# Kernel optimization log

Measured on AMD Instinct MI355X. Metric: run time of the kernel, lower is better.

Reference implementation:

```python
import jax, jax.numpy as jnp
import numpy as np
import math

ROPE_BASE = 10000.0
ALIBI_SLOPE = 2.0 ** (-8.0)  # _get_alibi_slopes(1) == [2**(-8*1/1)]


def _rope_cos_sin(T, d):
    inv_freq = 1.0 / (ROPE_BASE ** (jnp.arange(0, d, 2, dtype=jnp.float32) / d))
    t = jnp.arange(T, dtype=jnp.float32)
    freqs = jnp.einsum('i,j->ij', t, inv_freq)          # [T, d/2]
    emb = jnp.concatenate([freqs, freqs], axis=-1)      # [T, d]
    return jnp.cos(emb), jnp.sin(emb)


def _rotate_half(x):
    x1, x2 = jnp.split(x, 2, axis=-1)
    return jnp.concatenate([-x2, x1], axis=-1)


def setup_inputs() -> dict:
    key = jax.random.key(0)
    kq, kk, kv = jax.random.split(key, 3)
    B, T, H = 8, 2048, 256
    return {
        'q': jax.random.normal(kq, (B, T, H), dtype=jnp.float32),
        'k': jax.random.normal(kk, (B, T, H), dtype=jnp.float32),
        'v': jax.random.normal(kv, (B, T, H), dtype=jnp.float32),
    }


def reference(q, k, v):
    B, T, H = q.shape  # num_heads == 1, so head_dim == H
    cos, sin = _rope_cos_sin(T, H)                      # [T, H]
    qe = q * cos + _rotate_half(q) * sin                # [B, T, H]
    ke = k * cos + _rotate_half(k) * sin                # [B, T, H]

    scale = 1.0 / math.sqrt(H)
    scores = jnp.einsum('btd,bsd->bts', qe, ke) * scale  # [B, T, T]

    pos = jnp.arange(T)
    rel = (pos[None, :] - pos[:, None]).astype(jnp.float32)  # [T, T]
    alibi = (ALIBI_SLOPE * rel)[None, None, :, :]            # [1, 1, T, T]

    # torch broadcast: [B,T,T] + [1,1,T,T] -> [1,B,T,T]
    scores = scores + alibi
    attn = jax.nn.softmax(scores, axis=-1)              # [1, B, T, T]
    out = jnp.matmul(attn, v)                           # [1, B, T, H]
    return out
```

## Files before the change

### kernel.cpp

```cpp
#include <hip/hip_runtime.h>

#define B_ 8
#define T_ 2048
#define H_ 256
#define PSTR 40
#define SCALE2 0.0901684403f
#define SLOPE2 0.00563552752f
#define ELEMS ((size_t)B_ * T_ * H_)

typedef __attribute__((ext_vector_type(8))) short bf16x8;
typedef __attribute__((ext_vector_type(4))) float f32x4;

#define MFMA16(a, b, c) __builtin_amdgcn_mfma_f32_16x16x32_bf16((a), (b), (c), 0, 0, 0)

__device__ __forceinline__ ushort f2bf(float f) {
  unsigned u = __float_as_uint(f);
  u += 0x7FFFu + ((u >> 16) & 1u);
  return (ushort)(u >> 16);
}

__device__ __forceinline__ void gl_lds16(const ushort* g, ushort* l) {
  __builtin_amdgcn_global_load_lds(
      (const __attribute__((address_space(1))) unsigned int*)g,
      (__attribute__((address_space(3))) unsigned int*)l, 16, 0, 0);
}

__global__ void prep_kernel(const float* __restrict__ k, const float* __restrict__ v,
                            ushort* __restrict__ kt, ushort* __restrict__ vt) {
  __shared__ ushort tile[64][72];
  const int bid = blockIdx.x;
  const int tid = threadIdx.x;
  if (bid < 1024) {
    int idx = bid * 256 + tid;
    int d8 = idx & 15;
    int bt = idx >> 4;
    int t = bt & (T_ - 1);
    int b = bt >> 11;
    size_t base = (size_t)bt * H_ + d8 * 8;
    float4 a0 = *(const float4*)(k + base);
    float4 a1 = *(const float4*)(k + base + 4);
    float4 c0 = *(const float4*)(k + base + 128);
    float4 c1 = *(const float4*)(k + base + 132);
    float av[8] = {a0.x, a0.y, a0.z, a0.w, a1.x, a1.y, a1.z, a1.w};
    float cv[8] = {c0.x, c0.y, c0.z, c0.w, c1.x, c1.y, c1.z, c1.w};
    bf16x8 lo, hi;
#pragma unroll
    for (int e = 0; e < 8; ++e) {
      int j = d8 * 8 + e;
      float rv = (float)t * exp2f((float)j * -0.103810252959f) * 0.15915494309f;
      float fr = rv - floorf(rv);
      float sn = __builtin_amdgcn_sinf(fr), cs = __builtin_amdgcn_cosf(fr);
      lo[e] = (short)f2bf(av[e] * cs - cv[e] * sn);
      hi[e] = (short)f2bf(cv[e] * cs + av[e] * sn);
    }
    size_t kdst = (((size_t)(b * 64 + (t >> 5)) * 32 + d8) * 32 + (t & 31)) * 8;
    *(bf16x8*)(kt + kdst) = lo;
    *(bf16x8*)(kt + kdst + 4096) = hi;
  } else {
    int bid2 = bid - 1024;
    int b = bid2 >> 7, rem = bid2 & 127;
    int h0 = (rem >> 5) * 64, t0 = (rem & 31) * 64;
    int c4 = tid & 15, r0 = tid >> 4;
#pragma unroll
    for (int p = 0; p < 4; ++p) {
      int row = r0 + p * 16;
      const float4 f = *(const float4*)(v + ((size_t)(b * T_ + t0 + row)) * H_ + h0 + c4 * 4);
      ushort4 u;
      u.x = f2bf(f.x); u.y = f2bf(f.y); u.z = f2bf(f.z); u.w = f2bf(f.w);
      *(ushort4*)&tile[row][(c4 * 4) ^ (8 * ((row >> 3) & 7))] = u;
    }
    __syncthreads();
#pragma unroll
    for (int p = 0; p < 2; ++p) {
      int c = tid + p * 256;
      int h = c >> 3, tc = (c & 7) * 8;
      int xo = 8 * (c & 7);
      ushort4 u0, u1;
      u0.x = tile[tc + 0][h ^ xo]; u0.y = tile[tc + 1][h ^ xo];
      u0.z = tile[tc + 2][h ^ xo]; u0.w = tile[tc + 3][h ^ xo];
      u1.x = tile[tc + 4][h ^ xo]; u1.y = tile[tc + 5][h ^ xo];
      u1.z = tile[tc + 6][h ^ xo]; u1.w = tile[tc + 7][h ^ xo];
      int tg = t0 + tc;
      size_t dst = (((size_t)(b * 64 + (tg >> 5)) * 4 + ((tg >> 3) & 3)) * 256 + (h0 + h)) * 8;
      *(ushort4*)(vt + dst) = u0;
      *(ushort4*)(vt + dst + 4) = u1;
    }
  }
}

__global__ __launch_bounds__(256, 2)
void attn_kernel(const float* __restrict__ q, const ushort* __restrict__ kt,
                 const ushort* __restrict__ vt, float* __restrict__ out,
                 float* __restrict__ opart, float* __restrict__ lpart) {
  __shared__ ushort Ksh[2][8192];
  __shared__ ushort Vsh[2][8192];
  __shared__ ushort Psh[4][32 * PSTR];

  const int tid = threadIdx.x;
  const int w = tid >> 6, lane = tid & 63, quad = lane >> 4, l16 = lane & 15;
  const int b = blockIdx.x;
  const int q0 = blockIdx.y * 128;
  const int sp = blockIdx.z;
  const int S = gridDim.z;
  const int niter = (T_ / 32) / S;
  const int kvb = sp * (T_ / S);

  bf16x8 aq[2][8];
  {
    const float* qb = q + ((size_t)(b * T_) + q0 + w * 32) * H_;
#pragma unroll
    for (int mt = 0; mt < 2; ++mt) {
      int t = q0 + w * 32 + mt * 16 + l16;
      float qv[8][8];
#pragma unroll
      for (int ks = 0; ks < 8; ++ks) {
        float4 x0 = *(const float4*)(qb + (size_t)(mt * 16 + l16) * H_ + ks * 32 + quad * 8);
        float4 x1 = *(const float4*)(qb + (size_t)(mt * 16 + l16) * H_ + ks * 32 + quad * 8 + 4);
        qv[ks][0] = x0.x; qv[ks][1] = x0.y; qv[ks][2] = x0.z; qv[ks][3] = x0.w;
        qv[ks][4] = x1.x; qv[ks][5] = x1.y; qv[ks][6] = x1.z; qv[ks][7] = x1.w;
      }
#pragma unroll
      for (int ks = 0; ks < 4; ++ks)
#pragma unroll
        for (int e = 0; e < 8; ++e) {
          int d = ks * 32 + quad * 8 + e;
          float rv = (float)t * exp2f((float)d * -0.103810252959f) * 0.15915494309f;
          float fr = rv - floorf(rv);
          float sn = __builtin_amdgcn_sinf(fr), cs = __builtin_amdgcn_cosf(fr);
          aq[mt][ks][e]     = (short)f2bf(qv[ks][e] * cs - qv[ks + 4][e] * sn);
          aq[mt][ks + 4][e] = (short)f2bf(qv[ks + 4][e] * cs + qv[ks][e] * sn);
        }
    }
  }

  const f32x4 fzero = {0.f, 0.f, 0.f, 0.f};
  f32x4 O[2][16], lac[2];
#pragma unroll
  for (int mt = 0; mt < 2; ++mt) {
    lac[mt] = fzero;
#pragma unroll
    for (int ht = 0; ht < 16; ++ht) O[mt][ht] = fzero;
  }
  bf16x8 vones;
#pragma unroll
  for (int i = 0; i < 8; ++i) vones[i] = (short)0x3F80;

  const ushort* ktb = kt + (size_t)(b * 64 + sp * niter) * 8192;
  const ushort* vtb = vt + (size_t)(b * 64 + sp * niter) * 8192;
  const int stoff = tid * 8;

#pragma unroll
  for (int tt = 0; tt < 2; ++tt) {
    const ushort* kg = ktb + (size_t)tt * 8192;
    const ushort* vg = vtb + (size_t)tt * 8192;
#pragma unroll
    for (int i = 0; i < 4; ++i) {
      gl_lds16(kg + stoff + i * 2048, &Ksh[tt][stoff + i * 2048]);
      gl_lds16(vg + stoff + i * 2048, &Vsh[tt][stoff + i * 2048]);
    }
  }

  const float arb = SLOPE2 * (float)(q0 + w * 32 + quad * 4);

  for (int it = 0; it < niter; ++it) {
    const int p = it & 1;
    __builtin_amdgcn_sched_barrier(0);
    if (it == niter - 1) __builtin_amdgcn_s_waitcnt(0x0070);
    else                 __builtin_amdgcn_s_waitcnt(0x0F78);
    __builtin_amdgcn_s_barrier();
    __builtin_amdgcn_sched_barrier(0);

    f32x4 s[2][2] = {{fzero, fzero}, {fzero, fzero}};
    __builtin_amdgcn_s_setprio(1);
#pragma unroll
    for (int ks = 0; ks < 8; ++ks)
#pragma unroll
      for (int nt = 0; nt < 2; ++nt) {
        bf16x8 kf = *(const bf16x8*)&Ksh[p][((ks * 4 + quad) * 32 + nt * 16 + l16) * 8];
        s[0][nt] = MFMA16(aq[0][ks], kf, s[0][nt]);
        s[1][nt] = MFMA16(aq[1][ks], kf, s[1][nt]);
      }
    __builtin_amdgcn_s_setprio(0);

#pragma unroll
    for (int nt = 0; nt < 2; ++nt) {
      float ac = SLOPE2 * (float)(kvb + it * 32 + nt * 16 + l16);
#pragma unroll
      for (int mt = 0; mt < 2; ++mt)
#pragma unroll
        for (int r = 0; r < 4; ++r) {
          float a0 = ac - arb - SLOPE2 * (float)(mt * 16 + r);
          float pv = __builtin_amdgcn_exp2f(fmaf(s[mt][nt][r], SCALE2, a0));
          Psh[w][(mt * 16 + quad * 4 + r) * PSTR + nt * 16 + l16] = f2bf(pv);
        }
    }

    bf16x8 pf0 = *(const bf16x8*)&Psh[w][l16 * PSTR + quad * 8];
    bf16x8 pf1 = *(const bf16x8*)&Psh[w][(16 + l16) * PSTR + quad * 8];
    __builtin_amdgcn_s_setprio(1);
    lac[0] = MFMA16(pf0, vones, lac[0]);
    lac[1] = MFMA16(pf1, vones, lac[1]);
#pragma unroll
    for (int ht = 0; ht < 16; ++ht) {
      bf16x8 vf = *(const bf16x8*)&Vsh[p][(quad * 256 + ht * 16 + l16) * 8];
      O[0][ht] = MFMA16(pf0, vf, O[0][ht]);
      O[1][ht] = MFMA16(pf1, vf, O[1][ht]);
    }
    __builtin_amdgcn_s_setprio(0);

    __builtin_amdgcn_sched_barrier(0);
    __builtin_amdgcn_s_waitcnt(0xC07F);
    __builtin_amdgcn_s_barrier();
    __builtin_amdgcn_sched_barrier(0);

    if (it < niter - 2) {
      const ushort* kg = ktb + (size_t)(it + 2) * 8192;
      const ushort* vg = vtb + (size_t)(it + 2) * 8192;
#pragma unroll
      for (int i = 0; i < 4; ++i) {
        gl_lds16(kg + stoff + i * 2048, &Ksh[p][stoff + i * 2048]);
        gl_lds16(vg + stoff + i * 2048, &Vsh[p][stoff + i * 2048]);
      }
    }
  }

  float* od = (sp == 0) ? out : (opart + (size_t)(sp - 1) * ELEMS);
  float* ob = od + ((size_t)(b * T_) + q0 + w * 32) * H_;
#pragma unroll
  for (int mt = 0; mt < 2; ++mt)
#pragma unroll
    for (int r = 0; r < 4; ++r) {
      int row = mt * 16 + quad * 4 + r;
#pragma unroll
      for (int ht = 0; ht < 16; ++ht)
        ob[(size_t)row * H_ + ht * 16 + l16] = O[mt][ht][r];
    }
  if (l16 == 0) {
#pragma unroll
    for (int mt = 0; mt < 2; ++mt)
#pragma unroll
      for (int r = 0; r < 4; ++r)
        lpart[(size_t)(sp * B_ + b) * T_ + q0 + w * 32 + mt * 16 + quad * 4 + r] =
            lac[mt][r];
  }
}

__global__ void combine_kernel(float* __restrict__ out, const float* __restrict__ opart,
                               const float* __restrict__ lpart, int S) {
  int idx = blockIdx.x * 256 + threadIdx.x;
  int row = idx >> 6;
  float l = lpart[row];
  for (int s = 1; s < S; ++s) l += lpart[(size_t)s * B_ * T_ + row];
  float inv = 1.0f / l;
  float4 a = ((const float4*)out)[idx];
  for (int s = 1; s < S; ++s) {
    float4 c = ((const float4*)opart)[(size_t)(s - 1) * (ELEMS / 4) + idx];
    a.x += c.x; a.y += c.y; a.z += c.z; a.w += c.w;
  }
  a.x *= inv; a.y *= inv; a.z *= inv; a.w *= inv;
  ((float4*)out)[idx] = a;
}

extern "C" void kernel_launch(void* const* d_in, const int* in_sizes, int n_in,
                              void* d_out, int out_size, void* d_ws, size_t ws_size,
                              hipStream_t stream) {
  const float* q = (const float*)d_in[0];
  const float* k = (const float*)d_in[1];
  const float* v = (const float*)d_in[2];
  float* out = (float*)d_out;

  ushort* kt = (ushort*)d_ws;
  ushort* vt = kt + ELEMS;
  float* opart = (float*)(vt + ELEMS);
  const size_t need4 = ELEMS * 4 + 3 * ELEMS * 4 + (size_t)4 * B_ * T_ * 4;
  const int S = (ws_size >= need4) ? 4 : 2;
  float* lpart = opart + (size_t)(S - 1) * ELEMS;

  prep_kernel<<<dim3(2048), 256, 0, stream>>>(k, v, kt, vt);
  attn_kernel<<<dim3(B_, T_ / 128, S), 256, 0, stream>>>(q, kt, vt, out, opart, lpart);
  combine_kernel<<<dim3((B_ * T_ * H_ / 4) / 256), 256, 0, stream>>>(out, opart, lpart, S);
}
```

Before: 152.3 us.

## Software-pipeline QK^T one tile ahead of softmax/PV and fix split to two

Restructures the attention loop so that the QK^T MFMAs for tile it are issued in the same iteration as the exp/PV work for tile it-1, using a triple-buffered V tile in LDS so V stays resident one extra iteration. The KV split is hardcoded to 2 (down from 4 when workspace allowed), which shrinks the combine pass and partial-output traffic but halves grid parallelism. Launch bounds drop to 1 block per CU to give the extra live accumulators registers, and setprio hints are removed. The risk is reduced occupancy and fewer blocks (256 total) hurting latency hiding on a 256-CU part.

```diff
diff --git a/kernel.cpp b/kernel.cpp
--- a/kernel.cpp
+++ b/kernel.cpp
@@ -88,12 +88,12 @@
   }
 }
 
-__global__ __launch_bounds__(256, 2)
+__global__ __launch_bounds__(256, 1)
 void attn_kernel(const float* __restrict__ q, const ushort* __restrict__ kt,
                  const ushort* __restrict__ vt, float* __restrict__ out,
-                 float* __restrict__ opart, float* __restrict__ lpart) {
+                 float* __restrict__ o1, float* __restrict__ lpart) {
   __shared__ ushort Ksh[2][8192];
-  __shared__ ushort Vsh[2][8192];
+  __shared__ ushort Vsh[3][8192];
   __shared__ ushort Psh[4][32 * PSTR];
 
   const int tid = threadIdx.x;
@@ -101,9 +101,7 @@
   const int b = blockIdx.x;
   const int q0 = blockIdx.y * 128;
   const int sp = blockIdx.z;
-  const int S = gridDim.z;
-  const int niter = (T_ / 32) / S;
-  const int kvb = sp * (T_ / S);
+  const int kvb = sp * (T_ / 2);
 
   bf16x8 aq[2][8];
   {
@@ -145,8 +143,8 @@
 #pragma unroll
   for (int i = 0; i < 8; ++i) vones[i] = (short)0x3F80;
 
-  const ushort* ktb = kt + (size_t)(b * 64 + sp * niter) * 8192;
-  const ushort* vtb = vt + (size_t)(b * 64 + sp * niter) * 8192;
+  const ushort* ktb = kt + (size_t)(b * 64 + sp * 32) * 8192;
+  const ushort* vtb = vt + (size_t)(b * 64 + sp * 32) * 8192;
   const int stoff = tid * 8;
 
 #pragma unroll
@@ -161,70 +159,125 @@
   }
 
   const float arb = SLOPE2 * (float)(q0 + w * 32 + quad * 4);
-
-  for (int it = 0; it < niter; ++it) {
+  f32x4 s_prev[2][2] = {{fzero, fzero}, {fzero, fzero}};
+
+  {
+    __builtin_amdgcn_sched_barrier(0);
+    __builtin_amdgcn_s_waitcnt(0x0F78);
+    __builtin_amdgcn_s_barrier();
+    __builtin_amdgcn_sched_barrier(0);
+#pragma unroll
+    for (int ks = 0; ks < 8; ++ks)
+#pragma unroll
+      for (int nt = 0; nt < 2; ++nt) {
+        bf16x8 kf = *(const bf16x8*)&Ksh[0][((ks * 4 + quad) * 32 + nt * 16 + l16) * 8];
+        s_prev[0][nt] = MFMA16(aq[0][ks], kf, s_prev[0][nt]);
+        s_prev[1][nt] = MFMA16(aq[1][ks], kf, s_prev[1][nt]);
+      }
+    __builtin_amdgcn_sched_barrier(0);
+    __builtin_amdgcn_s_waitcnt(0xC07F);
+    __builtin_amdgcn_s_barrier();
+    __builtin_amdgcn_sched_barrier(0);
+    const ushort* kg = ktb + (size_t)2 * 8192;
+    const ushort* vg = vtb + (size_t)2 * 8192;
+#pragma unroll
+    for (int i = 0; i < 4; ++i) {
+      gl_lds16(kg + stoff + i * 2048, &Ksh[0][stoff + i * 2048]);
+      gl_lds16(vg + stoff + i * 2048, &Vsh[2][stoff + i * 2048]);
+    }
+  }
+
+  for (int it = 1; it < 32; ++it) {
     const int p = it & 1;
-    __builtin_amdgcn_sched_barrier(0);
-    if (it == niter - 1) __builtin_amdgcn_s_waitcnt(0x0070);
-    else                 __builtin_amdgcn_s_waitcnt(0x0F78);
+    const int vp = (it - 1) % 3;
+    __builtin_amdgcn_sched_barrier(0);
+    if (it == 31) __builtin_amdgcn_s_waitcnt(0x0070);
+    else          __builtin_amdgcn_s_waitcnt(0x0F78);
     __builtin_amdgcn_s_barrier();
     __builtin_amdgcn_sched_barrier(0);
 
-    f32x4 s[2][2] = {{fzero, fzero}, {fzero, fzero}};
-    __builtin_amdgcn_s_setprio(1);
+    f32x4 s_cur[2][2] = {{fzero, fzero}, {fzero, fzero}};
 #pragma unroll
     for (int ks = 0; ks < 8; ++ks)
 #pragma unroll
       for (int nt = 0; nt < 2; ++nt) {
         bf16x8 kf = *(const bf16x8*)&Ksh[p][((ks * 4 + quad) * 32 + nt * 16 + l16) * 8];
-        s[0][nt] = MFMA16(aq[0][ks], kf, s[0][nt]);
-        s[1][nt] = MFMA16(aq[1][ks], kf, s[1][nt]);
+        s_cur[0][nt] = MFMA16(aq[0][ks], kf, s_cur[0][nt]);
+        s_cur[1][nt] = MFMA16(aq[1][ks], kf, s_cur[1][nt]);
       }
-    __builtin_amdgcn_s_setprio(0);
 
 #pragma unroll
     for (int nt = 0; nt < 2; ++nt) {
-      float ac = SLOPE2 * (float)(kvb + it * 32 + nt * 16 + l16);
+      float ac = SLOPE2 * (float)(kvb + (it - 1) * 32 + nt * 16 + l16);
 #pragma unroll
       for (int mt = 0; mt < 2; ++mt)
 #pragma unroll
         for (int r = 0; r < 4; ++r) {
           float a0 = ac - arb - SLOPE2 * (float)(mt * 16 + r);
-          float pv = __builtin_amdgcn_exp2f(fmaf(s[mt][nt][r], SCALE2, a0));
+          float pv = __builtin_amdgcn_exp2f(fmaf(s_prev[mt][nt][r], SCALE2, a0));
           Psh[w][(mt * 16 + quad * 4 + r) * PSTR + nt * 16 + l16] = f2bf(pv);
         }
     }
 
     bf16x8 pf0 = *(const bf16x8*)&Psh[w][l16 * PSTR + quad * 8];
     bf16x8 pf1 = *(const bf16x8*)&Psh[w][(16 + l16) * PSTR + quad * 8];
-    __builtin_amdgcn_s_setprio(1);
     lac[0] = MFMA16(pf0, vones, lac[0]);
     lac[1] = MFMA16(pf1, vones, lac[1]);
 #pragma unroll
     for (int ht = 0; ht < 16; ++ht) {
-      bf16x8 vf = *(const bf16x8*)&Vsh[p][(quad * 256 + ht * 16 + l16) * 8];
+      bf16x8 vf = *(const bf16x8*)&Vsh[vp][(quad * 256 + ht * 16 + l16) * 8];
       O[0][ht] = MFMA16(pf0, vf, O[0][ht]);
       O[1][ht] = MFMA16(pf1, vf, O[1][ht]);
     }
-    __builtin_amdgcn_s_setprio(0);
+
+#pragma unroll
+    for (int mt = 0; mt < 2; ++mt)
+#pragma unroll
+      for (int nt = 0; nt < 2; ++nt) s_prev[mt][nt] = s_cur[mt][nt];
 
     __builtin_amdgcn_sched_barrier(0);
     __builtin_amdgcn_s_waitcnt(0xC07F);
     __builtin_amdgcn_s_barrier();
     __builtin_amdgcn_sched_barrier(0);
 
-    if (it < niter - 2) {
+    if (it <= 29) {
       const ushort* kg = ktb + (size_t)(it + 2) * 8192;
       const ushort* vg = vtb + (size_t)(it + 2) * 8192;
+      ushort* vd = &Vsh[(it + 2) % 3][0];
 #pragma unroll
       for (int i = 0; i < 4; ++i) {
         gl_lds16(kg + stoff + i * 2048, &Ksh[p][stoff + i * 2048]);
-        gl_lds16(vg + stoff + i * 2048, &Vsh[p][stoff + i * 2048]);
+        gl_lds16(vg + stoff + i * 2048, vd + stoff + i * 2048);
       }
     }
   }
 
-  float* od = (sp == 0) ? out : (opart + (size_t)(sp - 1) * ELEMS);
+  {
+#pragma unroll
+    for (int nt = 0; nt < 2; ++nt) {
+      float ac = SLOPE2 * (float)(kvb + 31 * 32 + nt * 16 + l16);
+#pragma unroll
+      for (int mt = 0; mt < 2; ++mt)
+#pragma unroll
+        for (int r = 0; r < 4; ++r) {
+          float a0 = ac - arb - SLOPE2 * (float)(mt * 16 + r);
+          float pv = __builtin_amdgcn_exp2f(fmaf(s_prev[mt][nt][r], SCALE2, a0));
+          Psh[w][(mt * 16 + quad * 4 + r) * PSTR + nt * 16 + l16] = f2bf(pv);
+        }
+    }
+    bf16x8 pf0 = *(const bf16x8*)&Psh[w][l16 * PSTR + quad * 8];
+    bf16x8 pf1 = *(const bf16x8*)&Psh[w][(16 + l16) * PSTR + quad * 8];
+    lac[0] = MFMA16(pf0, vones, lac[0]);
+    lac[1] = MFMA16(pf1, vones, lac[1]);
+#pragma unroll
+    for (int ht = 0; ht < 16; ++ht) {
+      bf16x8 vf = *(const bf16x8*)&Vsh[1][(quad * 256 + ht * 16 + l16) * 8];
+      O[0][ht] = MFMA16(pf0, vf, O[0][ht]);
+      O[1][ht] = MFMA16(pf1, vf, O[1][ht]);
+    }
+  }
+
+  float* od = (sp == 0) ? out : o1;
   float* ob = od + ((size_t)(b * T_) + q0 + w * 32) * H_;
 #pragma unroll
   for (int mt = 0; mt < 2; ++mt)
@@ -242,22 +295,18 @@
       for (int r = 0; r < 4; ++r)
         lpart[(size_t)(sp * B_ + b) * T_ + q0 + w * 32 + mt * 16 + quad * 4 + r] =
             lac[mt][r];
-  }
-}
-
-__global__ void combine_kernel(float* __restrict__ out, const float* __restrict__ opart,
-                               const float* __restrict__ lpart, int S) {
+    }
+}
+
+__global__ void combine_kernel(float* __restrict__ out, const float* __restrict__ o1,
+                               const float* __restrict__ lpart) {
   int idx = blockIdx.x * 256 + threadIdx.x;
   int row = idx >> 6;
-  float l = lpart[row];
-  for (int s = 1; s < S; ++s) l += lpart[(size_t)s * B_ * T_ + row];
-  float inv = 1.0f / l;
+  float inv = 1.0f / (lpart[row] + lpart[B_ * T_ + row]);
   float4 a = ((const float4*)out)[idx];
-  for (int s = 1; s < S; ++s) {
-    float4 c = ((const float4*)opart)[(size_t)(s - 1) * (ELEMS / 4) + idx];
-    a.x += c.x; a.y += c.y; a.z += c.z; a.w += c.w;
-  }
-  a.x *= inv; a.y *= inv; a.z *= inv; a.w *= inv;
+  float4 c = ((const float4*)o1)[idx];
+  a.x = (a.x + c.x) * inv; a.y = (a.y + c.y) * inv;
+  a.z = (a.z + c.z) * inv; a.w = (a.w + c.w) * inv;
   ((float4*)out)[idx] = a;
 }
 
@@ -271,12 +320,10 @@
 
   ushort* kt = (ushort*)d_ws;
   ushort* vt = kt + ELEMS;
-  float* opart = (float*)(vt + ELEMS);
-  const size_t need4 = ELEMS * 4 + 3 * ELEMS * 4 + (size_t)4 * B_ * T_ * 4;
-  const int S = (ws_size >= need4) ? 4 : 2;
-  float* lpart = opart + (size_t)(S - 1) * ELEMS;
+  float* o1 = (float*)(vt + ELEMS);
+  float* lpart = o1 + ELEMS;
 
   prep_kernel<<<dim3(2048), 256, 0, stream>>>(k, v, kt, vt);
-  attn_kernel<<<dim3(B_, T_ / 128, S), 256, 0, stream>>>(q, kt, vt, out, opart, lpart);
-  combine_kernel<<<dim3((B_ * T_ * H_ / 4) / 256), 256, 0, stream>>>(out, opart, lpart, S);
-}
+  attn_kernel<<<dim3(B_, T_ / 128, 2), 256, 0, stream>>>(q, kt, vt, out, o1, lpart);
+  combine_kernel<<<dim3((B_ * T_ * H_ / 4) / 256), 256, 0, stream>>>(out, o1, lpart);
+}
```

Measured after the change: 169.9 us. 11.5% more time.

## Use 8 waves of 16 query rows per block instead of 4 waves of 32

Applied to the files above, without the earlier changes.

Restructures the attention kernel so each block runs 512 threads, with each wave owning 16 query rows rather than 32. This halves per-wave accumulator and Q-fragment registers and raises the launch bound to 4 blocks per CU. Each thread now issues half as many K/V async loads per tile, and the waitcnt and setprio hints are adjusted to match. In exchange, every K fragment read from LDS feeds only one MFMA instead of two, so LDS traffic per FLOP doubles, and more waves share each barrier.

```diff
diff --git a/kernel.cpp b/kernel.cpp
--- a/kernel.cpp
+++ b/kernel.cpp
@@ -88,13 +88,13 @@
   }
 }
 
-__global__ __launch_bounds__(256, 2)
+__global__ __launch_bounds__(512, 4)
 void attn_kernel(const float* __restrict__ q, const ushort* __restrict__ kt,
                  const ushort* __restrict__ vt, float* __restrict__ out,
                  float* __restrict__ opart, float* __restrict__ lpart) {
   __shared__ ushort Ksh[2][8192];
   __shared__ ushort Vsh[2][8192];
-  __shared__ ushort Psh[4][32 * PSTR];
+  __shared__ ushort Psh[8][16 * PSTR];
 
   const int tid = threadIdx.x;
   const int w = tid >> 6, lane = tid & 63, quad = lane >> 4, l16 = lane & 15;
@@ -105,42 +105,35 @@
   const int niter = (T_ / 32) / S;
   const int kvb = sp * (T_ / S);
 
-  bf16x8 aq[2][8];
+  bf16x8 aq[8];
   {
-    const float* qb = q + ((size_t)(b * T_) + q0 + w * 32) * H_;
-#pragma unroll
-    for (int mt = 0; mt < 2; ++mt) {
-      int t = q0 + w * 32 + mt * 16 + l16;
-      float qv[8][8];
-#pragma unroll
-      for (int ks = 0; ks < 8; ++ks) {
-        float4 x0 = *(const float4*)(qb + (size_t)(mt * 16 + l16) * H_ + ks * 32 + quad * 8);
-        float4 x1 = *(const float4*)(qb + (size_t)(mt * 16 + l16) * H_ + ks * 32 + quad * 8 + 4);
-        qv[ks][0] = x0.x; qv[ks][1] = x0.y; qv[ks][2] = x0.z; qv[ks][3] = x0.w;
-        qv[ks][4] = x1.x; qv[ks][5] = x1.y; qv[ks][6] = x1.z; qv[ks][7] = x1.w;
+    const float* qb = q + ((size_t)(b * T_) + q0 + w * 16) * H_;
+    const int t = q0 + w * 16 + l16;
+    float qv[8][8];
+#pragma unroll
+    for (int ks = 0; ks < 8; ++ks) {
+      float4 x0 = *(const float4*)(qb + (size_t)l16 * H_ + ks * 32 + quad * 8);
+      float4 x1 = *(const float4*)(qb + (size_t)l16 * H_ + ks * 32 + quad * 8 + 4);
+      qv[ks][0] = x0.x; qv[ks][1] = x0.y; qv[ks][2] = x0.z; qv[ks][3] = x0.w;
+      qv[ks][4] = x1.x; qv[ks][5] = x1.y; qv[ks][6] = x1.z; qv[ks][7] = x1.w;
+    }
+#pragma unroll
+    for (int ks = 0; ks < 4; ++ks)
+#pragma unroll
+      for (int e = 0; e < 8; ++e) {
+        int d = ks * 32 + quad * 8 + e;
+        float rv = (float)t * exp2f((float)d * -0.103810252959f) * 0.15915494309f;
+        float fr = rv - floorf(rv);
+        float sn = __builtin_amdgcn_sinf(fr), cs = __builtin_amdgcn_cosf(fr);
+        aq[ks][e]     = (short)f2bf(qv[ks][e] * cs - qv[ks + 4][e] * sn);
+        aq[ks + 4][e] = (short)f2bf(qv[ks + 4][e] * cs + qv[ks][e] * sn);
       }
-#pragma unroll
-      for (int ks = 0; ks < 4; ++ks)
-#pragma unroll
-        for (int e = 0; e < 8; ++e) {
-          int d = ks * 32 + quad * 8 + e;
-          float rv = (float)t * exp2f((float)d * -0.103810252959f) * 0.15915494309f;
-          float fr = rv - floorf(rv);
-          float sn = __builtin_amdgcn_sinf(fr), cs = __builtin_amdgcn_cosf(fr);
-          aq[mt][ks][e]     = (short)f2bf(qv[ks][e] * cs - qv[ks + 4][e] * sn);
-          aq[mt][ks + 4][e] = (short)f2bf(qv[ks + 4][e] * cs + qv[ks][e] * sn);
-        }
-    }
   }
 
   const f32x4 fzero = {0.f, 0.f, 0.f, 0.f};
-  f32x4 O[2][16], lac[2];
-#pragma unroll
-  for (int mt = 0; mt < 2; ++mt) {
-    lac[mt] = fzero;
-#pragma unroll
-    for (int ht = 0; ht < 16; ++ht) O[mt][ht] = fzero;
-  }
+  f32x4 O[16], lac = fzero;
+#pragma unroll
+  for (int ht = 0; ht < 16; ++ht) O[ht] = fzero;
   bf16x8 vones;
 #pragma unroll
   for (int i = 0; i < 8; ++i) vones[i] = (short)0x3F80;
@@ -153,60 +146,49 @@
   for (int tt = 0; tt < 2; ++tt) {
     const ushort* kg = ktb + (size_t)tt * 8192;
     const ushort* vg = vtb + (size_t)tt * 8192;
-#pragma unroll
-    for (int i = 0; i < 4; ++i) {
-      gl_lds16(kg + stoff + i * 2048, &Ksh[tt][stoff + i * 2048]);
-      gl_lds16(vg + stoff + i * 2048, &Vsh[tt][stoff + i * 2048]);
-    }
-  }
-
-  const float arb = SLOPE2 * (float)(q0 + w * 32 + quad * 4);
+    gl_lds16(kg + stoff, &Ksh[tt][stoff]);
+    gl_lds16(kg + stoff + 4096, &Ksh[tt][stoff + 4096]);
+    gl_lds16(vg + stoff, &Vsh[tt][stoff]);
+    gl_lds16(vg + stoff + 4096, &Vsh[tt][stoff + 4096]);
+  }
+
+  const float arb = SLOPE2 * (float)(q0 + w * 16 + quad * 4);
 
   for (int it = 0; it < niter; ++it) {
     const int p = it & 1;
     __builtin_amdgcn_sched_barrier(0);
     if (it == niter - 1) __builtin_amdgcn_s_waitcnt(0x0070);
-    else                 __builtin_amdgcn_s_waitcnt(0x0F78);
+    else                 __builtin_amdgcn_s_waitcnt(0x0F74);
     __builtin_amdgcn_s_barrier();
     __builtin_amdgcn_sched_barrier(0);
 
-    f32x4 s[2][2] = {{fzero, fzero}, {fzero, fzero}};
-    __builtin_amdgcn_s_setprio(1);
+    f32x4 s[2] = {fzero, fzero};
 #pragma unroll
     for (int ks = 0; ks < 8; ++ks)
 #pragma unroll
       for (int nt = 0; nt < 2; ++nt) {
         bf16x8 kf = *(const bf16x8*)&Ksh[p][((ks * 4 + quad) * 32 + nt * 16 + l16) * 8];
-        s[0][nt] = MFMA16(aq[0][ks], kf, s[0][nt]);
-        s[1][nt] = MFMA16(aq[1][ks], kf, s[1][nt]);
+        s[nt] = MFMA16(aq[ks], kf, s[nt]);
       }
-    __builtin_amdgcn_s_setprio(0);
 
 #pragma unroll
     for (int nt = 0; nt < 2; ++nt) {
       float ac = SLOPE2 * (float)(kvb + it * 32 + nt * 16 + l16);
 #pragma unroll
-      for (int mt = 0; mt < 2; ++mt)
-#pragma unroll
-        for (int r = 0; r < 4; ++r) {
-          float a0 = ac - arb - SLOPE2 * (float)(mt * 16 + r);
-          float pv = __builtin_amdgcn_exp2f(fmaf(s[mt][nt][r], SCALE2, a0));
-          Psh[w][(mt * 16 + quad * 4 + r) * PSTR + nt * 16 + l16] = f2bf(pv);
-        }
-    }
-
-    bf16x8 pf0 = *(const bf16x8*)&Psh[w][l16 * PSTR + quad * 8];
-    bf16x8 pf1 = *(const bf16x8*)&Psh[w][(16 + l16) * PSTR + quad * 8];
-    __builtin_amdgcn_s_setprio(1);
-    lac[0] = MFMA16(pf0, vones, lac[0]);
-    lac[1] = MFMA16(pf1, vones, lac[1]);
+      for (int r = 0; r < 4; ++r) {
+        float a0 = ac - arb - SLOPE2 * (float)r;
+        float pv = __builtin_amdgcn_exp2f(fmaf(s[nt][r], SCALE2, a0));
+        Psh[w][(quad * 4 + r) * PSTR + nt * 16 + l16] = f2bf(pv);
+      }
+    }
+
+    bf16x8 pf = *(const bf16x8*)&Psh[w][l16 * PSTR + quad * 8];
+    lac = MFMA16(pf, vones, lac);
 #pragma unroll
     for (int ht = 0; ht < 16; ++ht) {
       bf16x8 vf = *(const bf16x8*)&Vsh[p][(quad * 256 + ht * 16 + l16) * 8];
-      O[0][ht] = MFMA16(pf0, vf, O[0][ht]);
-      O[1][ht] = MFMA16(pf1, vf, O[1][ht]);
-    }
-    __builtin_amdgcn_s_setprio(0);
+      O[ht] = MFMA16(pf, vf, O[ht]);
+    }
 
     __builtin_amdgcn_sched_barrier(0);
     __builtin_amdgcn_s_waitcnt(0xC07F);
@@ -216,32 +198,26 @@
     if (it < niter - 2) {
       const ushort* kg = ktb + (size_t)(it + 2) * 8192;
       const ushort* vg = vtb + (size_t)(it + 2) * 8192;
-#pragma unroll
-      for (int i = 0; i < 4; ++i) {
-        gl_lds16(kg + stoff + i * 2048, &Ksh[p][stoff + i * 2048]);
-        gl_lds16(vg + stoff + i * 2048, &Vsh[p][stoff + i * 2048]);
-      }
+      gl_lds16(kg + stoff, &Ksh[p][stoff]);
+      gl_lds16(kg + stoff + 4096, &Ksh[p][stoff + 4096]);
+      gl_lds16(vg + stoff, &Vsh[p][stoff]);
+      gl_lds16(vg + stoff + 4096, &Vsh[p][stoff + 4096]);
     }
   }
 
   float* od = (sp == 0) ? out : (opart + (size_t)(sp - 1) * ELEMS);
-  float* ob = od + ((size_t)(b * T_) + q0 + w * 32) * H_;
-#pragma unroll
-  for (int mt = 0; mt < 2; ++mt)
-#pragma unroll
-    for (int r = 0; r < 4; ++r) {
-      int row = mt * 16 + quad * 4 + r;
-#pragma unroll
-      for (int ht = 0; ht < 16; ++ht)
-        ob[(size_t)row * H_ + ht * 16 + l16] = O[mt][ht][r];
-    }
+  float* ob = od + ((size_t)(b * T_) + q0 + w * 16) * H_;
+#pragma unroll
+  for (int r = 0; r < 4; ++r) {
+    int row = quad * 4 + r;
+#pragma unroll
+    for (int ht = 0; ht < 16; ++ht)
+      ob[(size_t)row * H_ + ht * 16 + l16] = O[ht][r];
+  }
   if (l16 == 0) {
 #pragma unroll
-    for (int mt = 0; mt < 2; ++mt)
-#pragma unroll
-      for (int r = 0; r < 4; ++r)
-        lpart[(size_t)(sp * B_ + b) * T_ + q0 + w * 32 + mt * 16 + quad * 4 + r] =
-            lac[mt][r];
+    for (int r = 0; r < 4; ++r)
+      lpart[(size_t)(sp * B_ + b) * T_ + q0 + w * 16 + quad * 4 + r] = lac[r];
   }
 }
 
@@ -277,6 +253,6 @@
   float* lpart = opart + (size_t)(S - 1) * ELEMS;
 
   prep_kernel<<<dim3(2048), 256, 0, stream>>>(k, v, kt, vt);
-  attn_kernel<<<dim3(B_, T_ / 128, S), 256, 0, stream>>>(q, kt, vt, out, opart, lpart);
+  attn_kernel<<<dim3(B_, T_ / 128, S), 512, 0, stream>>>(q, kt, vt, out, opart, lpart);
   combine_kernel<<<dim3((B_ * T_ * H_ / 4) / 256), 256, 0, stream>>>(out, opart, lpart, S);
 }
```

Result: no change. 153.4 us (+0.7%).
